# Kernel optimization log

Hardware: AMD Instinct MI355X
Metric: run time of the kernel (lower is better)

## Reference

```python
import jax, jax.numpy as jnp
import numpy as np

N_NODES = 100000


def gcn_conv(x, W, b, src, dst, num_nodes):
    """PyG GCNConv: out = D^{-1/2} (A + I) D^{-1/2} (x W) + b, messages src->dst."""
    h = x @ W  # [N, out]
    # degree with self-loops (edge weight 1)
    deg = jax.ops.segment_sum(jnp.ones(src.shape[0], dtype=x.dtype), dst,
                              num_segments=num_nodes) + 1.0
    dinv = jax.lax.rsqrt(deg)  # [N]
    norm = dinv[src] * dinv[dst]  # [E]
    msg = h[src] * norm[:, None]  # gather + scale, [E, out]
    agg = jax.ops.segment_sum(msg, dst, num_segments=num_nodes)
    # self-loop term: norm_ii = dinv[i]^2
    agg = agg + h * (dinv * dinv)[:, None]
    return agg + b


def setup_inputs() -> dict:
    key = jax.random.key(0)
    ks = jax.random.split(key, 9)
    N, F_in, H1, H2, C = N_NODES, 128, 64, 32, 10
    E = 3200000
    feature = jax.random.normal(ks[0], (N, F_in), dtype=jnp.float32)
    edge_index = jax.random.randint(ks[1], (2, E), 0, N, dtype=jnp.int64)
    def glorot(k, shape):
        lim = np.sqrt(6.0 / (shape[0] + shape[1]))
        return jax.random.uniform(k, shape, jnp.float32, -lim, lim)
    return {
        "feature": feature,
        "edge_index": edge_index,
        "W1": glorot(ks[2], (F_in, H1)),
        "b1": jnp.zeros((H1,), jnp.float32),
        "W2": glorot(ks[3], (H1, H2)),
        "b2": jnp.zeros((H2,), jnp.float32),
        "Wc": glorot(ks[4], (H2, C)),
        "bc": jnp.zeros((C,), jnp.float32),
    }


def reference(feature, edge_index, W1, b1, W2, b2, Wc, bc):
    src, dst = edge_index[0], edge_index[1]
    x = gcn_conv(feature, W1, b1, src, dst, N_NODES)
    x = jax.nn.relu(x)
    # dropout is identity in eval mode
    x = gcn_conv(x, W2, b2, src, dst, N_NODES)
    x = jax.nn.relu(x)
    logits = x @ Wc + bc
    return jax.nn.log_softmax(logits, axis=1)
```

## Files before the change

### kernel.cpp

```cpp
#include <hip/hip_runtime.h>

#define N_NODES 100000
#define F_IN 128
#define H1 64
#define H2 32
#define NCLS 10

#define BS_N 256
#define NBUCK ((N_NODES + BS_N - 1) / BS_N)
#define LCAP 32
#define MCAP 9216
#define OVCAP 6144
#define STCAP 9216
#define BIN_WG 256

typedef _Float16 h2_t __attribute__((ext_vector_type(2)));
typedef _Float16 f16x8 __attribute__((ext_vector_type(8)));
typedef float f32x4 __attribute__((ext_vector_type(4)));

__device__ __forceinline__ float fdot2u(unsigned int u, h2_t sel, float c) {
    return __builtin_amdgcn_fdot2(__builtin_bit_cast(h2_t, u), sel, c, false);
}
__device__ __forceinline__ void accd4(float* a, uint4 v, h2_t lo, h2_t hi) {
    a[0] = fdot2u(v.x, lo, a[0]); a[1] = fdot2u(v.x, hi, a[1]);
    a[2] = fdot2u(v.y, lo, a[2]); a[3] = fdot2u(v.y, hi, a[3]);
    a[4] = fdot2u(v.z, lo, a[4]); a[5] = fdot2u(v.z, hi, a[5]);
    a[6] = fdot2u(v.w, lo, a[6]); a[7] = fdot2u(v.w, hi, a[7]);
}
__device__ __forceinline__ unsigned int pkh(float a, float b) {
    return __builtin_bit_cast(unsigned int, __builtin_amdgcn_cvt_pkrtz(a, b));
}

__global__ __launch_bounds__(512) void bin_kernel(const int* __restrict__ src,
                                                  const int* __restrict__ dst, int E,
                                                  unsigned int* __restrict__ gcur,
                                                  unsigned int* __restrict__ mainr,
                                                  unsigned int* __restrict__ ovcnt,
                                                  unsigned int* __restrict__ ovbuf) {
    __shared__ unsigned int buf[NBUCK][LCAP + 1];
    __shared__ int cnt[NBUCK];
    int tid = threadIdx.x;
    for (int b = tid; b < NBUCK; b += 512) cnt[b] = 0;

    int chunk = (E + gridDim.x - 1) / gridDim.x;
    int e_lo = blockIdx.x * chunk;
    int e_hi = min(e_lo + chunk, E);

    int d[4], s[4];
    #pragma unroll
    for (int k = 0; k < 4; ++k) {
        int e = e_lo + k * 512 + tid;
        d[k] = 0; s[k] = 0;
        if (e < e_hi) { d[k] = dst[e]; s[k] = src[e]; }
    }
    __syncthreads();

    for (int base = e_lo; base < e_hi; base += 2048) {
        #pragma unroll
        for (int k = 0; k < 4; ++k) {
            if (base + k * 512 + tid < e_hi) {
                int b = d[k] >> 8;
                unsigned int en = ((unsigned int)s[k] << 8) | (unsigned int)(d[k] & 255);
                int p = atomicAdd(&cnt[b], 1);
                if (p < LCAP) buf[b][p] = en;
                else {
                    unsigned int op = atomicAdd(&ovcnt[b * 16], 1u);
                    if (op < OVCAP) ovbuf[(size_t)b * OVCAP + op] = en;
                }
            }
        }
        __syncthreads();
        {
            int nb = base + 2048;
            #pragma unroll
            for (int k = 0; k < 4; ++k) {
                int e = nb + k * 512 + tid;
                if (e < e_hi) { d[k] = dst[e]; s[k] = src[e]; }
            }
        }
        for (int b = tid; b < NBUCK; b += 512) {
            int c = cnt[b]; if (c > LCAP) c = LCAP;
            int nf = c & ~15;
            if (nf) {
                unsigned int gb = atomicAdd(&gcur[b * 16], (unsigned int)nf);
                if (gb + (unsigned)nf <= MCAP) {
                    for (int k = 0; k < nf; k += 4) {
                        uint4 v = make_uint4(buf[b][k], buf[b][k + 1],
                                             buf[b][k + 2], buf[b][k + 3]);
                        *(uint4*)&mainr[(size_t)b * MCAP + gb + k] = v;
                    }
                } else {
                    unsigned int op = atomicAdd(&ovcnt[b * 16], (unsigned int)nf);
                    for (int k = 0; k < nf; ++k)
                        if (op + k < OVCAP) ovbuf[(size_t)b * OVCAP + op + k] = buf[b][k];
                }
                int rem = c - nf;
                for (int k = 0; k < rem; ++k) buf[b][k] = buf[b][nf + k];
                cnt[b] = rem;
            } else {
                cnt[b] = c;
            }
        }
        __syncthreads();
    }
    for (int b = tid; b < NBUCK; b += 512) {
        int c = cnt[b]; if (c > LCAP) c = LCAP;
        int nf = c & ~3;
        if (nf) {
            unsigned int gb = atomicAdd(&gcur[b * 16], (unsigned int)nf);
            if (gb + (unsigned)nf <= MCAP) {
                for (int k = 0; k < nf; k += 4) {
                    uint4 v = make_uint4(buf[b][k], buf[b][k + 1],
                                         buf[b][k + 2], buf[b][k + 3]);
                    *(uint4*)&mainr[(size_t)b * MCAP + gb + k] = v;
                }
            } else {
                unsigned int op = atomicAdd(&ovcnt[b * 16], (unsigned int)nf);
                for (int k = 0; k < nf; ++k)
                    if (op + k < OVCAP) ovbuf[(size_t)b * OVCAP + op + k] = buf[b][k];
            }
        }
        int rem = c - nf;
        if (rem) {
            unsigned int ob = atomicAdd(&ovcnt[b * 16], (unsigned int)rem);
            for (int k = 0; k < rem; ++k)
                if (ob + k < OVCAP) ovbuf[(size_t)b * OVCAP + ob + k] = buf[b][nf + k];
        }
    }
}

__global__ __launch_bounds__(512) void build_kernel(const unsigned int* __restrict__ gcur,
                                                    unsigned int* __restrict__ mainr,
                                                    const unsigned int* __restrict__ ovcnt,
                                                    const unsigned int* __restrict__ ovbuf,
                                                    float* __restrict__ dinv,
                                                    int2* __restrict__ row_se) {
    __shared__ unsigned int stage[STCAP];
    __shared__ unsigned int outb[STCAP];
    __shared__ int degl[BS_N];
    __shared__ int rs_l[BS_N];
    __shared__ int curl[BS_N];
    __shared__ int wtot[4];
    int b = blockIdx.x;
    int tid = threadIdx.x;

    int cm = (int)gcur[b * 16]; if (cm > MCAP) cm = MCAP;
    for (int i = tid; i < cm; i += 512) stage[i] = mainr[(size_t)b * MCAP + i];
    int co = (int)ovcnt[b * 16]; if (co > OVCAP) co = OVCAP;
    for (int i = tid; i < co; i += 512) {
        int p = cm + i;
        if (p < STCAP) stage[p] = ovbuf[(size_t)b * OVCAP + i];
    }
    int c = cm + co; if (c > STCAP) c = STCAP;
    if (tid < BS_N) degl[tid] = 0;
    __syncthreads();

    for (int i = tid; i < c; i += 512) atomicAdd(&degl[stage[i] & 255], 1);
    __syncthreads();

    if (tid < BS_N) {
        int lane = tid & 63, w = tid >> 6;
        int d = degl[tid];
        int x = d;
        #pragma unroll
        for (int off = 1; off < 64; off <<= 1) {
            int y = __shfl_up(x, off);
            if (lane >= off) x += y;
        }
        if (lane == 63) wtot[w] = x;
        __syncthreads();
        int pbase = 0;
        #pragma unroll
        for (int k = 0; k < 4; ++k) if (k < w) pbase += wtot[k];
        rs_l[tid] = pbase + x - d;
        curl[tid] = 0;
    } else {
        __syncthreads();
    }
    __syncthreads();

    for (int i = tid; i < c; i += 512) {
        unsigned int en = stage[i];
        int dl = en & 255;
        int p = atomicAdd(&curl[dl], 1);
        outb[rs_l[dl] + p] = en >> 8;
    }
    __syncthreads();
    size_t gbase = (size_t)b * MCAP;
    int c4 = (c + 3) >> 2;
    for (int i = tid; i < c4; i += 512)
        *(uint4*)&mainr[gbase + (size_t)i * 4] = *(const uint4*)&outb[i * 4];

    int node = b * BS_N + tid;
    if (tid < BS_N && node < N_NODES) {
        int deg = degl[tid];
        dinv[node] = rsqrtf((float)deg + 1.0f);
        int rs = (int)gbase + rs_l[tid];
        row_se[node] = make_int2(rs, rs + deg);
    }
}

__global__ __launch_bounds__(256) void gemm1_kernel(const float* __restrict__ X,
                                                    const float* __restrict__ W,
                                                    const float* __restrict__ dinv,
                                                    unsigned short* __restrict__ H) {
    __shared__ union {
        struct {
            _Float16 As[64][136];
            _Float16 Wf[16][64][8];
        } s;
        _Float16 Hs[64][72];
    } u;
    int r0 = blockIdx.x * 64;
    int tid = threadIdx.x;
    for (int i = tid; i < 2048; i += 256) {
        int row = i >> 5, k4 = i & 31;
        int grow = r0 + row;
        float4 v = (grow < N_NODES) ? ((const float4*)X)[(size_t)grow * 32 + k4]
                                    : make_float4(0.f, 0.f, 0.f, 0.f);
        _Float16 t4[4] = {(_Float16)v.x, (_Float16)v.y, (_Float16)v.z, (_Float16)v.w};
        *(uint2*)&u.s.As[row][k4 * 4] = *(uint2*)t4;
    }
    for (int i = tid; i < F_IN * H1; i += 256) {
        int k = i >> 6, col = i & 63;
        u.s.Wf[k >> 3][col][k & 7] = (_Float16)W[i];
    }
    __syncthreads();

    int lane = tid & 63, w = tid >> 6;
    int lr = lane & 15, lkg = lane >> 4;
    f32x4 acc[4] = {{0.f, 0.f, 0.f, 0.f}, {0.f, 0.f, 0.f, 0.f},
                    {0.f, 0.f, 0.f, 0.f}, {0.f, 0.f, 0.f, 0.f}};
    #pragma unroll
    for (int ks = 0; ks < 4; ++ks) {
        f16x8 a = *(const f16x8*)&u.s.As[w * 16 + lr][ks * 32 + lkg * 8];
        #pragma unroll
        for (int nt = 0; nt < 4; ++nt) {
            f16x8 bfr = *(const f16x8*)&u.s.Wf[ks * 4 + lkg][nt * 16 + lr][0];
            acc[nt] = __builtin_amdgcn_mfma_f32_16x16x32_f16(a, bfr, acc[nt], 0, 0, 0);
        }
    }
    __syncthreads();
    float dv[4];
    #pragma unroll
    for (int q = 0; q < 4; ++q) {
        int grow = r0 + w * 16 + lkg * 4 + q;
        dv[q] = (grow < N_NODES) ? dinv[grow] : 0.f;
    }
    #pragma unroll
    for (int nt = 0; nt < 4; ++nt)
        #pragma unroll
        for (int q = 0; q < 4; ++q)
            u.Hs[w * 16 + lkg * 4 + q][nt * 16 + lr] = (_Float16)(acc[nt][q] * dv[q]);
    __syncthreads();
    for (int i = tid; i < 512; i += 256) {
        int row = i >> 3, seg = i & 7;
        int grow = r0 + row;
        if (grow < N_NODES)
            *(uint4*)&H[(size_t)grow * H1 + seg * 8] = *(const uint4*)&u.Hs[row][seg * 8];
    }
}

__global__ __launch_bounds__(256) void gemm2_kernel(const float* __restrict__ X,
                                                    const float* __restrict__ W,
                                                    const float* __restrict__ dinv,
                                                    unsigned short* __restrict__ H) {
    __shared__ float Xs[64][68];
    __shared__ float Ws[H1 * H2];
    int r0 = blockIdx.x * 64;
    const float4* W4 = (const float4*)W;
    float4* Ws4 = (float4*)Ws;
    for (int i = threadIdx.x; i < H1 * H2 / 4; i += 256) Ws4[i] = W4[i];
    for (int it = 0; it < 4; ++it) {
        int idx = threadIdx.x + it * 256;
        int r = idx >> 4, k4 = idx & 15;
        int row = r0 + r;
        float4 v = (row < N_NODES)
            ? ((const float4*)X)[(size_t)row * 16 + k4]
            : make_float4(0.f, 0.f, 0.f, 0.f);
        *(float4*)&Xs[r][k4 * 4] = v;
    }
    __syncthreads();
    int tx = threadIdx.x & 15;
    int ty = threadIdx.x >> 4;
    float acc[4][2] = {};
    #pragma unroll 8
    for (int k = 0; k < 64; ++k) {
        float2 wb = *(const float2*)&Ws[k * H2 + tx * 2];
        float xa0 = Xs[ty * 4 + 0][k];
        float xa1 = Xs[ty * 4 + 1][k];
        float xa2 = Xs[ty * 4 + 2][k];
        float xa3 = Xs[ty * 4 + 3][k];
        acc[0][0] += xa0 * wb.x; acc[0][1] += xa0 * wb.y;
        acc[1][0] += xa1 * wb.x; acc[1][1] += xa1 * wb.y;
        acc[2][0] += xa2 * wb.x; acc[2][1] += xa2 * wb.y;
        acc[3][0] += xa3 * wb.x; acc[3][1] += xa3 * wb.y;
    }
    #pragma unroll
    for (int i = 0; i < 4; ++i) {
        int row = r0 + ty * 4 + i;
        if (row < N_NODES) {
            float dv = dinv[row];
            *(unsigned int*)&H[(size_t)row * H2 + tx * 2] = pkh(acc[i][0] * dv, acc[i][1] * dv);
        }
    }
}

__global__ __launch_bounds__(256) void pull1_kernel(const unsigned short* __restrict__ h,
                                                    const unsigned int* __restrict__ csr,
                                                    const int2* __restrict__ row_se,
                                                    const float* __restrict__ dinv,
                                                    const float* __restrict__ b,
                                                    float* __restrict__ xout) {
    int wave = (blockIdx.x * 256 + threadIdx.x) >> 6;
    int lane = threadIdx.x & 63;
    int g = lane >> 3;
    int sub = lane & 7;
    int i = wave;
    int2 se = row_se[i];
    int e0 = se.x, e1 = se.y;
    int deg = e1 - e0;
    const h2_t selo = {(_Float16)1.0f, (_Float16)0.0f};
    const h2_t sehi = {(_Float16)0.0f, (_Float16)1.0f};
    float acc[8] = {};
    if (deg <= 48) {
        int sidx = (int)csr[e0 + lane];
        int i0 = __shfl(sidx, g);
        int i1 = __shfl(sidx, 8 + g);
        int i2 = __shfl(sidx, 16 + g);
        int i3 = __shfl(sidx, 24 + g);
        int i4 = __shfl(sidx, 32 + g);
        int i5 = __shfl(sidx, 40 + g);
        bool p0 = (g < deg),      p1 = (8 + g < deg),  p2 = (16 + g < deg);
        bool p3 = (24 + g < deg), p4 = (32 + g < deg), p5 = (40 + g < deg);
        uint4 v0 = make_uint4(0u, 0u, 0u, 0u), v1 = v0, v2 = v0, v3 = v0, v4 = v0, v5 = v0;
        if (p0) v0 = *(const uint4*)&h[(size_t)i0 * H1 + sub * 8];
        if (p1) v1 = *(const uint4*)&h[(size_t)i1 * H1 + sub * 8];
        if (p2) v2 = *(const uint4*)&h[(size_t)i2 * H1 + sub * 8];
        if (p3) v3 = *(const uint4*)&h[(size_t)i3 * H1 + sub * 8];
        if (p4) v4 = *(const uint4*)&h[(size_t)i4 * H1 + sub * 8];
        if (p5) v5 = *(const uint4*)&h[(size_t)i5 * H1 + sub * 8];
        if (p0) accd4(acc, v0, selo, sehi);
        if (p1) accd4(acc, v1, selo, sehi);
        if (p2) accd4(acc, v2, selo, sehi);
        if (p3) accd4(acc, v3, selo, sehi);
        if (p4) accd4(acc, v4, selo, sehi);
        if (p5) accd4(acc, v5, selo, sehi);
    } else {
        int e = e0;
        for (; e + 16 <= e1; e += 16) {
            int s0 = csr[e + g];
            int s1 = csr[e + 8 + g];
            uint4 v0 = *(const uint4*)&h[(size_t)s0 * H1 + sub * 8];
            uint4 v1 = *(const uint4*)&h[(size_t)s1 * H1 + sub * 8];
            accd4(acc, v0, selo, sehi);
            accd4(acc, v1, selo, sehi);
        }
        if (e + 8 <= e1) {
            int s = csr[e + g];
            uint4 v = *(const uint4*)&h[(size_t)s * H1 + sub * 8];
            accd4(acc, v, selo, sehi);
            e += 8;
        }
        if (e < e1) {
            int idx = e + g;
            if (idx < e1) {
                int s = csr[idx];
                uint4 v = *(const uint4*)&h[(size_t)s * H1 + sub * 8];
                accd4(acc, v, selo, sehi);
            }
        }
    }
    #pragma unroll
    for (int m = 8; m < 64; m <<= 1) {
        #pragma unroll
        for (int j = 0; j < 8; ++j) acc[j] += __shfl_xor(acc[j], m);
    }
    if (g == 0) {
        float di = dinv[i];
        uint4 sv = *(const uint4*)&h[(size_t)i * H1 + sub * 8];
        accd4(acc, sv, selo, sehi);
        float4 bb0 = *(const float4*)&b[sub * 8];
        float4 bb1 = *(const float4*)&b[sub * 8 + 4];
        float4 o0, o1;
        o0.x = fmaxf(di * acc[0] + bb0.x, 0.0f);
        o0.y = fmaxf(di * acc[1] + bb0.y, 0.0f);
        o0.z = fmaxf(di * acc[2] + bb0.z, 0.0f);
        o0.w = fmaxf(di * acc[3] + bb0.w, 0.0f);
        o1.x = fmaxf(di * acc[4] + bb1.x, 0.0f);
        o1.y = fmaxf(di * acc[5] + bb1.y, 0.0f);
        o1.z = fmaxf(di * acc[6] + bb1.z, 0.0f);
        o1.w = fmaxf(di * acc[7] + bb1.w, 0.0f);
        *(float4*)&xout[(size_t)i * H1 + sub * 8] = o0;
        *(float4*)&xout[(size_t)i * H1 + sub * 8 + 4] = o1;
    }
}

__global__ __launch_bounds__(256) void pull2_kernel(const unsigned short* __restrict__ h,
                                                    const unsigned int* __restrict__ csr,
                                                    const int2* __restrict__ row_se,
                                                    const float* __restrict__ dinv,
                                                    const float* __restrict__ b,
                                                    float* __restrict__ xout) {
    int wave = (blockIdx.x * 256 + threadIdx.x) >> 6;
    int lane = threadIdx.x & 63;
    int g = lane >> 2;
    int sub = lane & 3;
    int i = wave;
    int2 se = row_se[i];
    int e0 = se.x, e1 = se.y;
    int deg = e1 - e0;
    const h2_t selo = {(_Float16)1.0f, (_Float16)0.0f};
    const h2_t sehi = {(_Float16)0.0f, (_Float16)1.0f};
    float acc[8] = {};
    if (deg <= 48) {
        int sidx = (int)csr[e0 + lane];
        int i0 = __shfl(sidx, g);
        int i1 = __shfl(sidx, 16 + g);
        int i2 = __shfl(sidx, 32 + g);
        bool p0 = (g < deg), p1 = (16 + g < deg), p2 = (32 + g < deg);
        uint4 v0 = make_uint4(0u, 0u, 0u, 0u), v1 = v0, v2 = v0;
        if (p0) v0 = *(const uint4*)&h[(size_t)i0 * H2 + sub * 8];
        if (p1) v1 = *(const uint4*)&h[(size_t)i1 * H2 + sub * 8];
        if (p2) v2 = *(const uint4*)&h[(size_t)i2 * H2 + sub * 8];
        if (p0) accd4(acc, v0, selo, sehi);
        if (p1) accd4(acc, v1, selo, sehi);
        if (p2) accd4(acc, v2, selo, sehi);
    } else {
        int e = e0;
        for (; e + 32 <= e1; e += 32) {
            int s0 = csr[e + g];
            int s1 = csr[e + 16 + g];
            uint4 v0 = *(const uint4*)&h[(size_t)s0 * H2 + sub * 8];
            uint4 v1 = *(const uint4*)&h[(size_t)s1 * H2 + sub * 8];
            accd4(acc, v0, selo, sehi);
            accd4(acc, v1, selo, sehi);
        }
        if (e + 16 <= e1) {
            int s = csr[e + g];
            uint4 v = *(const uint4*)&h[(size_t)s * H2 + sub * 8];
            accd4(acc, v, selo, sehi);
            e += 16;
        }
        if (e < e1) {
            int idx = e + g;
            if (idx < e1) {
                int s = csr[idx];
                uint4 v = *(const uint4*)&h[(size_t)s * H2 + sub * 8];
                accd4(acc, v, selo, sehi);
            }
        }
    }
    #pragma unroll
    for (int m = 4; m < 64; m <<= 1) {
        #pragma unroll
        for (int j = 0; j < 8; ++j) acc[j] += __shfl_xor(acc[j], m);
    }
    if (g == 0) {
        float di = dinv[i];
        uint4 sv = *(const uint4*)&h[(size_t)i * H2 + sub * 8];
        accd4(acc, sv, selo, sehi);
        float4 bb0 = *(const float4*)&b[sub * 8];
        float4 bb1 = *(const float4*)&b[sub * 8 + 4];
        float4 o0, o1;
        o0.x = fmaxf(di * acc[0] + bb0.x, 0.0f);
        o0.y = fmaxf(di * acc[1] + bb0.y, 0.0f);
        o0.z = fmaxf(di * acc[2] + bb0.z, 0.0f);
        o0.w = fmaxf(di * acc[3] + bb0.w, 0.0f);
        o1.x = fmaxf(di * acc[4] + bb1.x, 0.0f);
        o1.y = fmaxf(di * acc[5] + bb1.y, 0.0f);
        o1.z = fmaxf(di * acc[6] + bb1.z, 0.0f);
        o1.w = fmaxf(di * acc[7] + bb1.w, 0.0f);
        *(float4*)&xout[(size_t)i * H2 + sub * 8] = o0;
        *(float4*)&xout[(size_t)i * H2 + sub * 8 + 4] = o1;
    }
}

__global__ __launch_bounds__(256) void final_kernel(const float* __restrict__ X2,
                                                    const float* __restrict__ Wc,
                                                    const float* __restrict__ bc,
                                                    float* __restrict__ out) {
    __shared__ float Ws[H2 * NCLS];
    __shared__ float bs[NCLS];
    for (int idx = threadIdx.x; idx < H2 * NCLS; idx += 256) Ws[idx] = Wc[idx];
    if (threadIdx.x < NCLS) bs[threadIdx.x] = bc[threadIdx.x];
    __syncthreads();
    int i = blockIdx.x * blockDim.x + threadIdx.x;
    if (i >= N_NODES) return;
    float x[H2];
    #pragma unroll
    for (int k = 0; k < H2; ++k) x[k] = X2[(size_t)i * H2 + k];
    float lg[NCLS];
    #pragma unroll
    for (int c = 0; c < NCLS; ++c) {
        float acc = bs[c];
        #pragma unroll
        for (int k = 0; k < H2; ++k) acc += x[k] * Ws[k * NCLS + c];
        lg[c] = acc;
    }
    float m = lg[0];
    #pragma unroll
    for (int c = 1; c < NCLS; ++c) m = fmaxf(m, lg[c]);
    float s = 0.0f;
    #pragma unroll
    for (int c = 0; c < NCLS; ++c) s += expf(lg[c] - m);
    float lse = m + logf(s);
    #pragma unroll
    for (int c = 0; c < NCLS; ++c) out[(size_t)i * NCLS + c] = lg[c] - lse;
}

extern "C" void kernel_launch(void* const* d_in, const int* in_sizes, int n_in,
                              void* d_out, int out_size, void* d_ws, size_t ws_size,
                              hipStream_t stream) {
    const float* feature = (const float*)d_in[0];
    const int*   eidx    = (const int*)d_in[1];
    const float* W1      = (const float*)d_in[2];
    const float* b1      = (const float*)d_in[3];
    const float* W2      = (const float*)d_in[4];
    const float* b2      = (const float*)d_in[5];
    const float* Wc      = (const float*)d_in[6];
    const float* bc      = (const float*)d_in[7];
    float* out = (float*)d_out;

    const int E = in_sizes[1] / 2;
    const int* src = eidx;
    const int* dst = eidx + E;

    float*          ws        = (float*)d_ws;
    float*          dinv      = ws;
    int2*           row_se    = (int2*)(dinv + N_NODES);
    unsigned int*   gcur      = (unsigned int*)(row_se + N_NODES);
    unsigned int*   ovcnt     = gcur + (size_t)NBUCK * 16;
    unsigned int*   ovbuf     = ovcnt + (size_t)NBUCK * 16;
    unsigned int*   mainr     = ovbuf + (size_t)NBUCK * OVCAP;
    unsigned short* h1b       = (unsigned short*)(mainr + (size_t)NBUCK * MCAP);
    float*          x1        = (float*)(h1b + (size_t)N_NODES * H1);
    unsigned short* h2b       = h1b;
    float*          x2        = x1;

    hipMemsetAsync(gcur, 0, (size_t)NBUCK * 32 * sizeof(unsigned int), stream);
    bin_kernel<<<BIN_WG, 512, 0, stream>>>(src, dst, E, gcur, mainr, ovcnt, ovbuf);
    build_kernel<<<NBUCK, 512, 0, stream>>>(gcur, mainr, ovcnt, ovbuf, dinv, row_se);

    gemm1_kernel<<<(N_NODES + 63) / 64, 256, 0, stream>>>(feature, W1, dinv, h1b);
    {
        unsigned int grid = (unsigned int)(((size_t)N_NODES * 64 + 255) / 256);
        pull1_kernel<<<grid, 256, 0, stream>>>(h1b, mainr, row_se, dinv, b1, x1);
    }

    gemm2_kernel<<<(N_NODES + 63) / 64, 256, 0, stream>>>(x1, W2, dinv, h2b);
    {
        unsigned int grid = (unsigned int)(((size_t)N_NODES * 64 + 255) / 256);
        pull2_kernel<<<grid, 256, 0, stream>>>(h2b, mainr, row_se, dinv, b2, x2);
    }

    final_kernel<<<(N_NODES + 255) / 256, 256, 0, stream>>>(x2, Wc, bc, out);
}
```

Baseline: 272.8 us.

## Process two nodes per wave in pull1 and fuse classifier into pull2

pull1 now has each wavefront aggregate two destination nodes. It interleaves their neighbour gathers so more loads are in flight, and the grid is halved. pull2 absorbs the final linear layer and log-softmax: it stages each node's hidden vector in shared memory and computes the logits within the block. That removes the x2 write and reread and one kernel launch. The costs are extra block-level syncs and shared-memory traffic in pull2, and more register pressure in pull1.

```diff
diff --git a/kernel.cpp b/kernel.cpp
--- a/kernel.cpp
+++ b/kernel.cpp
@@ -306,6 +306,51 @@
     }
 }
 
+#define GEN1(e0v, e1v, acc) do {                                               \
+    int e = (e0v);                                                             \
+    for (; e + 16 <= (e1v); e += 16) {                                         \
+        int s0 = csr[e + g];                                                   \
+        int s1 = csr[e + 8 + g];                                               \
+        uint4 v0 = *(const uint4*)&h[(size_t)s0 * H1 + sub * 8];               \
+        uint4 v1 = *(const uint4*)&h[(size_t)s1 * H1 + sub * 8];               \
+        accd4(acc, v0, selo, sehi);                                            \
+        accd4(acc, v1, selo, sehi);                                            \
+    }                                                                          \
+    if (e + 8 <= (e1v)) {                                                      \
+        int s0 = csr[e + g];                                                   \
+        uint4 v0 = *(const uint4*)&h[(size_t)s0 * H1 + sub * 8];               \
+        accd4(acc, v0, selo, sehi);                                            \
+        e += 8;                                                                \
+    }                                                                          \
+    if (e < (e1v)) {                                                           \
+        int idx = e + g;                                                       \
+        if (idx < (e1v)) {                                                     \
+            int s0 = csr[idx];                                                 \
+            uint4 v0 = *(const uint4*)&h[(size_t)s0 * H1 + sub * 8];           \
+            accd4(acc, v0, selo, sehi);                                        \
+        }                                                                      \
+    }                                                                          \
+} while (0)
+
+#define EPI1(nodei, acc) do {                                                  \
+    float di = dinv[nodei];                                                    \
+    uint4 sv = *(const uint4*)&h[(size_t)(nodei) * H1 + sub * 8];              \
+    accd4(acc, sv, selo, sehi);                                                \
+    float4 bb0 = *(const float4*)&b[sub * 8];                                  \
+    float4 bb1 = *(const float4*)&b[sub * 8 + 4];                              \
+    float4 o0, o1;                                                             \
+    o0.x = fmaxf(di * (acc)[0] + bb0.x, 0.0f);                                 \
+    o0.y = fmaxf(di * (acc)[1] + bb0.y, 0.0f);                                 \
+    o0.z = fmaxf(di * (acc)[2] + bb0.z, 0.0f);                                 \
+    o0.w = fmaxf(di * (acc)[3] + bb0.w, 0.0f);                                 \
+    o1.x = fmaxf(di * (acc)[4] + bb1.x, 0.0f);                                 \
+    o1.y = fmaxf(di * (acc)[5] + bb1.y, 0.0f);                                 \
+    o1.z = fmaxf(di * (acc)[6] + bb1.z, 0.0f);                                 \
+    o1.w = fmaxf(di * (acc)[7] + bb1.w, 0.0f);                                 \
+    *(float4*)&xout[(size_t)(nodei) * H1 + sub * 8] = o0;                      \
+    *(float4*)&xout[(size_t)(nodei) * H1 + sub * 8 + 4] = o1;                  \
+} while (0)
+
 __global__ __launch_bounds__(256) void pull1_kernel(const unsigned short* __restrict__ h,
                                                     const unsigned int* __restrict__ csr,
                                                     const int2* __restrict__ row_se,
@@ -316,83 +361,67 @@
     int lane = threadIdx.x & 63;
     int g = lane >> 3;
     int sub = lane & 7;
-    int i = wave;
-    int2 se = row_se[i];
-    int e0 = se.x, e1 = se.y;
-    int deg = e1 - e0;
+    int iA = wave * 2, iB = iA + 1;
+    int4 se2 = *(const int4*)&row_se[iA];
+    int e0A = se2.x, e1A = se2.y, e0B = se2.z, e1B = se2.w;
+    int degA = e1A - e0A, degB = e1B - e0B;
     const h2_t selo = {(_Float16)1.0f, (_Float16)0.0f};
     const h2_t sehi = {(_Float16)0.0f, (_Float16)1.0f};
-    float acc[8] = {};
-    if (deg <= 48) {
-        int sidx = (int)csr[e0 + lane];
-        int i0 = __shfl(sidx, g);
-        int i1 = __shfl(sidx, 8 + g);
-        int i2 = __shfl(sidx, 16 + g);
-        int i3 = __shfl(sidx, 24 + g);
-        int i4 = __shfl(sidx, 32 + g);
-        int i5 = __shfl(sidx, 40 + g);
-        bool p0 = (g < deg),      p1 = (8 + g < deg),  p2 = (16 + g < deg);
-        bool p3 = (24 + g < deg), p4 = (32 + g < deg), p5 = (40 + g < deg);
-        uint4 v0 = make_uint4(0u, 0u, 0u, 0u), v1 = v0, v2 = v0, v3 = v0, v4 = v0, v5 = v0;
-        if (p0) v0 = *(const uint4*)&h[(size_t)i0 * H1 + sub * 8];
-        if (p1) v1 = *(const uint4*)&h[(size_t)i1 * H1 + sub * 8];
-        if (p2) v2 = *(const uint4*)&h[(size_t)i2 * H1 + sub * 8];
-        if (p3) v3 = *(const uint4*)&h[(size_t)i3 * H1 + sub * 8];
-        if (p4) v4 = *(const uint4*)&h[(size_t)i4 * H1 + sub * 8];
-        if (p5) v5 = *(const uint4*)&h[(size_t)i5 * H1 + sub * 8];
-        if (p0) accd4(acc, v0, selo, sehi);
-        if (p1) accd4(acc, v1, selo, sehi);
-        if (p2) accd4(acc, v2, selo, sehi);
-        if (p3) accd4(acc, v3, selo, sehi);
-        if (p4) accd4(acc, v4, selo, sehi);
-        if (p5) accd4(acc, v5, selo, sehi);
+    float accA[8] = {}, accB[8] = {};
+    if (degA <= 48 && degB <= 48) {
+        int sA = (int)csr[e0A + lane];
+        int sB = (int)csr[e0B + lane];
+        int a0 = __shfl(sA, g),      a1 = __shfl(sA, 8 + g),  a2 = __shfl(sA, 16 + g);
+        int a3 = __shfl(sA, 24 + g), a4 = __shfl(sA, 32 + g), a5 = __shfl(sA, 40 + g);
+        int b0 = __shfl(sB, g),      b1 = __shfl(sB, 8 + g),  b2 = __shfl(sB, 16 + g);
+        int b3 = __shfl(sB, 24 + g), b4 = __shfl(sB, 32 + g), b5 = __shfl(sB, 40 + g);
+        bool pa0 = (g < degA),      pa1 = (8 + g < degA),  pa2 = (16 + g < degA);
+        bool pa3 = (24 + g < degA), pa4 = (32 + g < degA), pa5 = (40 + g < degA);
+        bool pb0 = (g < degB),      pb1 = (8 + g < degB),  pb2 = (16 + g < degB);
+        bool pb3 = (24 + g < degB), pb4 = (32 + g < degB), pb5 = (40 + g < degB);
+        uint4 z = make_uint4(0u, 0u, 0u, 0u);
+        uint4 va0 = z, va1 = z, va2 = z, va3 = z, va4 = z, va5 = z;
+        uint4 vb0 = z, vb1 = z, vb2 = z, vb3 = z, vb4 = z, vb5 = z;
+        if (pa0) va0 = *(const uint4*)&h[(size_t)a0 * H1 + sub * 8];
+        if (pb0) vb0 = *(const uint4*)&h[(size_t)b0 * H1 + sub * 8];
+        if (pa1) va1 = *(const uint4*)&h[(size_t)a1 * H1 + sub * 8];
+        if (pb1) vb1 = *(const uint4*)&h[(size_t)b1 * H1 + sub * 8];
+        if (pa2) va2 = *(const uint4*)&h[(size_t)a2 * H1 + sub * 8];
+        if (pb2) vb2 = *(const uint4*)&h[(size_t)b2 * H1 + sub * 8];
+        if (pa3) va3 = *(const uint4*)&h[(size_t)a3 * H1 + sub * 8];
+        if (pb3) vb3 = *(const uint4*)&h[(size_t)b3 * H1 + sub * 8];
+        if (pa4) va4 = *(const uint4*)&h[(size_t)a4 * H1 + sub * 8];
+        if (pb4) vb4 = *(const uint4*)&h[(size_t)b4 * H1 + sub * 8];
+        if (pa5) va5 = *(const uint4*)&h[(size_t)a5 * H1 + sub * 8];
+        if (pb5) vb5 = *(const uint4*)&h[(size_t)b5 * H1 + sub * 8];
+        if (pa0) accd4(accA, va0, selo, sehi);
+        if (pa1) accd4(accA, va1, selo, sehi);
+        if (pa2) accd4(accA, va2, selo, sehi);
+        if (pa3) accd4(accA, va3, selo, sehi);
+        if (pa4) accd4(accA, va4, selo, sehi);
+        if (pa5) accd4(accA, va5, selo, sehi);
+        if (pb0) accd4(accB, vb0, selo, sehi);
+        if (pb1) accd4(accB, vb1, selo, sehi);
+        if (pb2) accd4(accB, vb2, selo, sehi);
+        if (pb3) accd4(accB, vb3, selo, sehi);
+        if (pb4) accd4(accB, vb4, selo, sehi);
+        if (pb5) accd4(accB, vb5, selo, sehi);
     } else {
-        int e = e0;
-        for (; e + 16 <= e1; e += 16) {
-            int s0 = csr[e + g];
-            int s1 = csr[e + 8 + g];
-            uint4 v0 = *(const uint4*)&h[(size_t)s0 * H1 + sub * 8];
-            uint4 v1 = *(const uint4*)&h[(size_t)s1 * H1 + sub * 8];
-            accd4(acc, v0, selo, sehi);
-            accd4(acc, v1, selo, sehi);
-        }
-        if (e + 8 <= e1) {
-            int s = csr[e + g];
-            uint4 v = *(const uint4*)&h[(size_t)s * H1 + sub * 8];
-            accd4(acc, v, selo, sehi);
-            e += 8;
-        }
-        if (e < e1) {
-            int idx = e + g;
-            if (idx < e1) {
-                int s = csr[idx];
-                uint4 v = *(const uint4*)&h[(size_t)s * H1 + sub * 8];
-                accd4(acc, v, selo, sehi);
-            }
-        }
+        GEN1(e0A, e1A, accA);
+        GEN1(e0B, e1B, accB);
     }
     #pragma unroll
     for (int m = 8; m < 64; m <<= 1) {
         #pragma unroll
-        for (int j = 0; j < 8; ++j) acc[j] += __shfl_xor(acc[j], m);
-    }
-    if (g == 0) {
-        float di = dinv[i];
-        uint4 sv = *(const uint4*)&h[(size_t)i * H1 + sub * 8];
-        accd4(acc, sv, selo, sehi);
-        float4 bb0 = *(const float4*)&b[sub * 8];
-        float4 bb1 = *(const float4*)&b[sub * 8 + 4];
-        float4 o0, o1;
-        o0.x = fmaxf(di * acc[0] + bb0.x, 0.0f);
-        o0.y = fmaxf(di * acc[1] + bb0.y, 0.0f);
-        o0.z = fmaxf(di * acc[2] + bb0.z, 0.0f);
-        o0.w = fmaxf(di * acc[3] + bb0.w, 0.0f);
-        o1.x = fmaxf(di * acc[4] + bb1.x, 0.0f);
-        o1.y = fmaxf(di * acc[5] + bb1.y, 0.0f);
-        o1.z = fmaxf(di * acc[6] + bb1.z, 0.0f);
-        o1.w = fmaxf(di * acc[7] + bb1.w, 0.0f);
-        *(float4*)&xout[(size_t)i * H1 + sub * 8] = o0;
-        *(float4*)&xout[(size_t)i * H1 + sub * 8 + 4] = o1;
+        for (int j = 0; j < 8; ++j) {
+            accA[j] += __shfl_xor(accA[j], m);
+            accB[j] += __shfl_xor(accB[j], m);
+        }
+    }
+    if (lane < 8) {
+        EPI1(iA, accA);
+    } else if (lane < 16) {
+        EPI1(iB, accB);
     }
 }
 
@@ -401,12 +430,24 @@
                                                     const int2* __restrict__ row_se,
                                                     const float* __restrict__ dinv,
                                                     const float* __restrict__ b,
-                                                    float* __restrict__ xout) {
-    int wave = (blockIdx.x * 256 + threadIdx.x) >> 6;
-    int lane = threadIdx.x & 63;
+                                                    const float* __restrict__ Wc,
+                                                    const float* __restrict__ bc,
+                                                    float* __restrict__ out) {
+    __shared__ float WsL[H2 * NCLS];
+    __shared__ float bsL[NCLS];
+    __shared__ float xsh[4][H2];
+    __shared__ float lgl[4][NCLS];
+    __shared__ float lsel[4];
+    int tid = threadIdx.x;
+    for (int idx = tid; idx < H2 * NCLS; idx += 256) WsL[idx] = Wc[idx];
+    if (tid < NCLS) bsL[tid] = bc[tid];
+    __syncthreads();
+
+    int w = tid >> 6;
+    int i = blockIdx.x * 4 + w;
+    int lane = tid & 63;
     int g = lane >> 2;
     int sub = lane & 3;
-    int i = wave;
     int2 se = row_se[i];
     int e0 = se.x, e1 = se.y;
     int deg = e1 - e0;
@@ -462,51 +503,38 @@
         accd4(acc, sv, selo, sehi);
         float4 bb0 = *(const float4*)&b[sub * 8];
         float4 bb1 = *(const float4*)&b[sub * 8 + 4];
-        float4 o0, o1;
-        o0.x = fmaxf(di * acc[0] + bb0.x, 0.0f);
-        o0.y = fmaxf(di * acc[1] + bb0.y, 0.0f);
-        o0.z = fmaxf(di * acc[2] + bb0.z, 0.0f);
-        o0.w = fmaxf(di * acc[3] + bb0.w, 0.0f);
-        o1.x = fmaxf(di * acc[4] + bb1.x, 0.0f);
-        o1.y = fmaxf(di * acc[5] + bb1.y, 0.0f);
-        o1.z = fmaxf(di * acc[6] + bb1.z, 0.0f);
-        o1.w = fmaxf(di * acc[7] + bb1.w, 0.0f);
-        *(float4*)&xout[(size_t)i * H2 + sub * 8] = o0;
-        *(float4*)&xout[(size_t)i * H2 + sub * 8 + 4] = o1;
-    }
-}
-
-__global__ __launch_bounds__(256) void final_kernel(const float* __restrict__ X2,
-                                                    const float* __restrict__ Wc,
-                                                    const float* __restrict__ bc,
-                                                    float* __restrict__ out) {
-    __shared__ float Ws[H2 * NCLS];
-    __shared__ float bs[NCLS];
-    for (int idx = threadIdx.x; idx < H2 * NCLS; idx += 256) Ws[idx] = Wc[idx];
-    if (threadIdx.x < NCLS) bs[threadIdx.x] = bc[threadIdx.x];
-    __syncthreads();
-    int i = blockIdx.x * blockDim.x + threadIdx.x;
-    if (i >= N_NODES) return;
-    float x[H2];
-    #pragma unroll
-    for (int k = 0; k < H2; ++k) x[k] = X2[(size_t)i * H2 + k];
-    float lg[NCLS];
-    #pragma unroll
-    for (int c = 0; c < NCLS; ++c) {
-        float acc = bs[c];
-        #pragma unroll
-        for (int k = 0; k < H2; ++k) acc += x[k] * Ws[k * NCLS + c];
-        lg[c] = acc;
-    }
-    float m = lg[0];
-    #pragma unroll
-    for (int c = 1; c < NCLS; ++c) m = fmaxf(m, lg[c]);
-    float s = 0.0f;
-    #pragma unroll
-    for (int c = 0; c < NCLS; ++c) s += expf(lg[c] - m);
-    float lse = m + logf(s);
-    #pragma unroll
-    for (int c = 0; c < NCLS; ++c) out[(size_t)i * NCLS + c] = lg[c] - lse;
+        xsh[w][sub * 8 + 0] = fmaxf(di * acc[0] + bb0.x, 0.0f);
+        xsh[w][sub * 8 + 1] = fmaxf(di * acc[1] + bb0.y, 0.0f);
+        xsh[w][sub * 8 + 2] = fmaxf(di * acc[2] + bb0.z, 0.0f);
+        xsh[w][sub * 8 + 3] = fmaxf(di * acc[3] + bb0.w, 0.0f);
+        xsh[w][sub * 8 + 4] = fmaxf(di * acc[4] + bb1.x, 0.0f);
+        xsh[w][sub * 8 + 5] = fmaxf(di * acc[5] + bb1.y, 0.0f);
+        xsh[w][sub * 8 + 6] = fmaxf(di * acc[6] + bb1.z, 0.0f);
+        xsh[w][sub * 8 + 7] = fmaxf(di * acc[7] + bb1.w, 0.0f);
+    }
+    __syncthreads();
+    if (tid < 4 * NCLS) {
+        int nd = tid / NCLS, c2 = tid % NCLS;
+        float a2 = bsL[c2];
+        #pragma unroll
+        for (int k = 0; k < H2; ++k) a2 += xsh[nd][k] * WsL[k * NCLS + c2];
+        lgl[nd][c2] = a2;
+    }
+    __syncthreads();
+    if (tid < 4) {
+        float m2 = lgl[tid][0];
+        #pragma unroll
+        for (int c2 = 1; c2 < NCLS; ++c2) m2 = fmaxf(m2, lgl[tid][c2]);
+        float s2 = 0.f;
+        #pragma unroll
+        for (int c2 = 0; c2 < NCLS; ++c2) s2 += expf(lgl[tid][c2] - m2);
+        lsel[tid] = m2 + logf(s2);
+    }
+    __syncthreads();
+    if (tid < 4 * NCLS) {
+        int nd = tid / NCLS, c2 = tid % NCLS;
+        out[(size_t)(blockIdx.x * 4 + nd) * NCLS + c2] = lgl[nd][c2] - lsel[nd];
+    }
 }
 
 extern "C" void kernel_launch(void* const* d_in, const int* in_sizes, int n_in,
@@ -536,23 +564,14 @@
     unsigned short* h1b       = (unsigned short*)(mainr + (size_t)NBUCK * MCAP);
     float*          x1        = (float*)(h1b + (size_t)N_NODES * H1);
     unsigned short* h2b       = h1b;
-    float*          x2        = x1;
 
     hipMemsetAsync(gcur, 0, (size_t)NBUCK * 32 * sizeof(unsigned int), stream);
     bin_kernel<<<BIN_WG, 512, 0, stream>>>(src, dst, E, gcur, mainr, ovcnt, ovbuf);
     build_kernel<<<NBUCK, 512, 0, stream>>>(gcur, mainr, ovcnt, ovbuf, dinv, row_se);
 
     gemm1_kernel<<<(N_NODES + 63) / 64, 256, 0, stream>>>(feature, W1, dinv, h1b);
-    {
-        unsigned int grid = (unsigned int)(((size_t)N_NODES * 64 + 255) / 256);
-        pull1_kernel<<<grid, 256, 0, stream>>>(h1b, mainr, row_se, dinv, b1, x1);
-    }
+    pull1_kernel<<<12500, 256, 0, stream>>>(h1b, mainr, row_se, dinv, b1, x1);
 
     gemm2_kernel<<<(N_NODES + 63) / 64, 256, 0, stream>>>(x1, W2, dinv, h2b);
-    {
-        unsigned int grid = (unsigned int)(((size_t)N_NODES * 64 + 255) / 256);
-        pull2_kernel<<<grid, 256, 0, stream>>>(h2b, mainr, row_se, dinv, b2, x2);
-    }
-
-    final_kernel<<<(N_NODES + 255) / 256, 256, 0, stream>>>(x2, Wc, bc, out);
-}
+    pull2_kernel<<<N_NODES / 4, 256, 0, stream>>>(h2b, mainr, row_se, dinv, b2, Wc, bc, out);
+}
```

Result: slower. 287.8 us (+5.5%).

## Split layer-2 pull aggregation into two source-range passes for cache locality

Applied to the files above, without the earlier changes.

The layer-2 gather-aggregate runs as two passes. Each pass gathers only neighbours whose source index falls in one half of the node range, so the gathered h rows for that half (about 3.2 MB in fp16) stay in cache. The first pass writes float partial sums to a new buffer, and the second pass adds them back before the bias, ReLU and scaling. In exchange every pass re-reads the CSR and row ranges, and a full fp32 partial tensor is written and read. The unrolled 32-edge loop is also replaced by a simpler 16-edge loop.

```diff
diff --git a/kernel.cpp b/kernel.cpp
--- a/kernel.cpp
+++ b/kernel.cpp
@@ -5,6 +5,7 @@
 #define H1 64
 #define H2 32
 #define NCLS 10
+#define SPLIT 50000
 
 #define BS_N 256
 #define NBUCK ((N_NODES + BS_N - 1) / BS_N)
@@ -396,12 +397,10 @@
     }
 }
 
-__global__ __launch_bounds__(256) void pull2_kernel(const unsigned short* __restrict__ h,
-                                                    const unsigned int* __restrict__ csr,
-                                                    const int2* __restrict__ row_se,
-                                                    const float* __restrict__ dinv,
-                                                    const float* __restrict__ b,
-                                                    float* __restrict__ xout) {
+__global__ __launch_bounds__(256) void pull2a_kernel(const unsigned short* __restrict__ h,
+                                                     const unsigned int* __restrict__ csr,
+                                                     const int2* __restrict__ row_se,
+                                                     float* __restrict__ part) {
     int wave = (blockIdx.x * 256 + threadIdx.x) >> 6;
     int lane = threadIdx.x & 63;
     int g = lane >> 2;
@@ -418,7 +417,9 @@
         int i0 = __shfl(sidx, g);
         int i1 = __shfl(sidx, 16 + g);
         int i2 = __shfl(sidx, 32 + g);
-        bool p0 = (g < deg), p1 = (16 + g < deg), p2 = (32 + g < deg);
+        bool p0 = (g < deg) && (i0 < SPLIT);
+        bool p1 = (16 + g < deg) && (i1 < SPLIT);
+        bool p2 = (32 + g < deg) && (i2 < SPLIT);
         uint4 v0 = make_uint4(0u, 0u, 0u, 0u), v1 = v0, v2 = v0;
         if (p0) v0 = *(const uint4*)&h[(size_t)i0 * H2 + sub * 8];
         if (p1) v1 = *(const uint4*)&h[(size_t)i1 * H2 + sub * 8];
@@ -427,27 +428,14 @@
         if (p1) accd4(acc, v1, selo, sehi);
         if (p2) accd4(acc, v2, selo, sehi);
     } else {
-        int e = e0;
-        for (; e + 32 <= e1; e += 32) {
-            int s0 = csr[e + g];
-            int s1 = csr[e + 16 + g];
-            uint4 v0 = *(const uint4*)&h[(size_t)s0 * H2 + sub * 8];
-            uint4 v1 = *(const uint4*)&h[(size_t)s1 * H2 + sub * 8];
-            accd4(acc, v0, selo, sehi);
-            accd4(acc, v1, selo, sehi);
-        }
-        if (e + 16 <= e1) {
-            int s = csr[e + g];
-            uint4 v = *(const uint4*)&h[(size_t)s * H2 + sub * 8];
-            accd4(acc, v, selo, sehi);
-            e += 16;
-        }
-        if (e < e1) {
+        for (int e = e0; e < e1; e += 16) {
             int idx = e + g;
             if (idx < e1) {
                 int s = csr[idx];
-                uint4 v = *(const uint4*)&h[(size_t)s * H2 + sub * 8];
-                accd4(acc, v, selo, sehi);
+                if (s < SPLIT) {
+                    uint4 v = *(const uint4*)&h[(size_t)s * H2 + sub * 8];
+                    accd4(acc, v, selo, sehi);
+                }
             }
         }
     }
@@ -457,9 +445,77 @@
         for (int j = 0; j < 8; ++j) acc[j] += __shfl_xor(acc[j], m);
     }
     if (g == 0) {
+        if (i < SPLIT) {
+            uint4 sv = *(const uint4*)&h[(size_t)i * H2 + sub * 8];
+            accd4(acc, sv, selo, sehi);
+        }
+        *(float4*)&part[(size_t)i * H2 + sub * 8] =
+            make_float4(acc[0], acc[1], acc[2], acc[3]);
+        *(float4*)&part[(size_t)i * H2 + sub * 8 + 4] =
+            make_float4(acc[4], acc[5], acc[6], acc[7]);
+    }
+}
+
+__global__ __launch_bounds__(256) void pull2b_kernel(const unsigned short* __restrict__ h,
+                                                     const unsigned int* __restrict__ csr,
+                                                     const int2* __restrict__ row_se,
+                                                     const float* __restrict__ dinv,
+                                                     const float* __restrict__ b,
+                                                     const float* __restrict__ part,
+                                                     float* __restrict__ xout) {
+    int wave = (blockIdx.x * 256 + threadIdx.x) >> 6;
+    int lane = threadIdx.x & 63;
+    int g = lane >> 2;
+    int sub = lane & 3;
+    int i = wave;
+    int2 se = row_se[i];
+    int e0 = se.x, e1 = se.y;
+    int deg = e1 - e0;
+    const h2_t selo = {(_Float16)1.0f, (_Float16)0.0f};
+    const h2_t sehi = {(_Float16)0.0f, (_Float16)1.0f};
+    float acc[8] = {};
+    if (deg <= 48) {
+        int sidx = (int)csr[e0 + lane];
+        int i0 = __shfl(sidx, g);
+        int i1 = __shfl(sidx, 16 + g);
+        int i2 = __shfl(sidx, 32 + g);
+        bool p0 = (g < deg) && (i0 >= SPLIT);
+        bool p1 = (16 + g < deg) && (i1 >= SPLIT);
+        bool p2 = (32 + g < deg) && (i2 >= SPLIT);
+        uint4 v0 = make_uint4(0u, 0u, 0u, 0u), v1 = v0, v2 = v0;
+        if (p0) v0 = *(const uint4*)&h[(size_t)i0 * H2 + sub * 8];
+        if (p1) v1 = *(const uint4*)&h[(size_t)i1 * H2 + sub * 8];
+        if (p2) v2 = *(const uint4*)&h[(size_t)i2 * H2 + sub * 8];
+        if (p0) accd4(acc, v0, selo, sehi);
+        if (p1) accd4(acc, v1, selo, sehi);
+        if (p2) accd4(acc, v2, selo, sehi);
+    } else {
+        for (int e = e0; e < e1; e += 16) {
+            int idx = e + g;
+            if (idx < e1) {
+                int s = csr[idx];
+                if (s >= SPLIT) {
+                    uint4 v = *(const uint4*)&h[(size_t)s * H2 + sub * 8];
+                    accd4(acc, v, selo, sehi);
+                }
+            }
+        }
+    }
+    #pragma unroll
+    for (int m = 4; m < 64; m <<= 1) {
+        #pragma unroll
+        for (int j = 0; j < 8; ++j) acc[j] += __shfl_xor(acc[j], m);
+    }
+    if (g == 0) {
+        if (i >= SPLIT) {
+            uint4 sv = *(const uint4*)&h[(size_t)i * H2 + sub * 8];
+            accd4(acc, sv, selo, sehi);
+        }
+        float4 pr0 = *(const float4*)&part[(size_t)i * H2 + sub * 8];
+        float4 pr1 = *(const float4*)&part[(size_t)i * H2 + sub * 8 + 4];
+        acc[0] += pr0.x; acc[1] += pr0.y; acc[2] += pr0.z; acc[3] += pr0.w;
+        acc[4] += pr1.x; acc[5] += pr1.y; acc[6] += pr1.z; acc[7] += pr1.w;
         float di = dinv[i];
-        uint4 sv = *(const uint4*)&h[(size_t)i * H2 + sub * 8];
-        accd4(acc, sv, selo, sehi);
         float4 bb0 = *(const float4*)&b[sub * 8];
         float4 bb1 = *(const float4*)&b[sub * 8 + 4];
         float4 o0, o1;
@@ -537,6 +593,7 @@
     float*          x1        = (float*)(h1b + (size_t)N_NODES * H1);
     unsigned short* h2b       = h1b;
     float*          x2        = x1;
+    float*          part      = x1 + (size_t)N_NODES * H2;
 
     hipMemsetAsync(gcur, 0, (size_t)NBUCK * 32 * sizeof(unsigned int), stream);
     bin_kernel<<<BIN_WG, 512, 0, stream>>>(src, dst, E, gcur, mainr, ovcnt, ovbuf);
@@ -551,7 +608,8 @@
     gemm2_kernel<<<(N_NODES + 63) / 64, 256, 0, stream>>>(x1, W2, dinv, h2b);
     {
         unsigned int grid = (unsigned int)(((size_t)N_NODES * 64 + 255) / 256);
-        pull2_kernel<<<grid, 256, 0, stream>>>(h2b, mainr, row_se, dinv, b2, x2);
+        pull2a_kernel<<<grid, 256, 0, stream>>>(h2b, mainr, row_se, part);
+        pull2b_kernel<<<grid, 256, 0, stream>>>(h2b, mainr, row_se, dinv, b2, part, x2);
     }
 
     final_kernel<<<(N_NODES + 255) / 256, 256, 0, stream>>>(x2, Wc, bc, out);
```

After: 314.5 us. 1.15x slower.

## Fuse layer-2 GEMM into layer-1 aggregation epilogue

Applied to the files above, without the earlier changes.

Removes the separate gemm2 kernel. The pull1 kernel now stages a transposed W2 in shared memory and, after aggregating each node, applies bias, ReLU, the 64x32 projection and dinv scaling, writing fp16 h2 directly. This avoids writing and re-reading the fp32 intermediate x1 and saves one launch. It costs redundant per-lane projection math, a per-block W2 load and an extra shuffle reduction in the aggregation kernel.

```diff
diff --git a/kernel.cpp b/kernel.cpp
--- a/kernel.cpp
+++ b/kernel.cpp
@@ -261,57 +261,20 @@
     }
 }
 
-__global__ __launch_bounds__(256) void gemm2_kernel(const float* __restrict__ X,
-                                                    const float* __restrict__ W,
-                                                    const float* __restrict__ dinv,
-                                                    unsigned short* __restrict__ H) {
-    __shared__ float Xs[64][68];
-    __shared__ float Ws[H1 * H2];
-    int r0 = blockIdx.x * 64;
-    const float4* W4 = (const float4*)W;
-    float4* Ws4 = (float4*)Ws;
-    for (int i = threadIdx.x; i < H1 * H2 / 4; i += 256) Ws4[i] = W4[i];
-    for (int it = 0; it < 4; ++it) {
-        int idx = threadIdx.x + it * 256;
-        int r = idx >> 4, k4 = idx & 15;
-        int row = r0 + r;
-        float4 v = (row < N_NODES)
-            ? ((const float4*)X)[(size_t)row * 16 + k4]
-            : make_float4(0.f, 0.f, 0.f, 0.f);
-        *(float4*)&Xs[r][k4 * 4] = v;
-    }
-    __syncthreads();
-    int tx = threadIdx.x & 15;
-    int ty = threadIdx.x >> 4;
-    float acc[4][2] = {};
-    #pragma unroll 8
-    for (int k = 0; k < 64; ++k) {
-        float2 wb = *(const float2*)&Ws[k * H2 + tx * 2];
-        float xa0 = Xs[ty * 4 + 0][k];
-        float xa1 = Xs[ty * 4 + 1][k];
-        float xa2 = Xs[ty * 4 + 2][k];
-        float xa3 = Xs[ty * 4 + 3][k];
-        acc[0][0] += xa0 * wb.x; acc[0][1] += xa0 * wb.y;
-        acc[1][0] += xa1 * wb.x; acc[1][1] += xa1 * wb.y;
-        acc[2][0] += xa2 * wb.x; acc[2][1] += xa2 * wb.y;
-        acc[3][0] += xa3 * wb.x; acc[3][1] += xa3 * wb.y;
-    }
-    #pragma unroll
-    for (int i = 0; i < 4; ++i) {
-        int row = r0 + ty * 4 + i;
-        if (row < N_NODES) {
-            float dv = dinv[row];
-            *(unsigned int*)&H[(size_t)row * H2 + tx * 2] = pkh(acc[i][0] * dv, acc[i][1] * dv);
-        }
-    }
-}
-
 __global__ __launch_bounds__(256) void pull1_kernel(const unsigned short* __restrict__ h,
                                                     const unsigned int* __restrict__ csr,
                                                     const int2* __restrict__ row_se,
                                                     const float* __restrict__ dinv,
                                                     const float* __restrict__ b,
-                                                    float* __restrict__ xout) {
+                                                    const float* __restrict__ W2,
+                                                    unsigned short* __restrict__ h2out) {
+    __shared__ float W2t[H2 * H1];
+    for (int idx = threadIdx.x; idx < H1 * H2; idx += 256) {
+        int k = idx >> 5, c = idx & 31;
+        W2t[c * H1 + k] = W2[idx];
+    }
+    __syncthreads();
+
     int wave = (blockIdx.x * 256 + threadIdx.x) >> 6;
     int lane = threadIdx.x & 63;
     int g = lane >> 3;
@@ -376,23 +339,37 @@
         #pragma unroll
         for (int j = 0; j < 8; ++j) acc[j] += __shfl_xor(acc[j], m);
     }
-    if (g == 0) {
-        float di = dinv[i];
-        uint4 sv = *(const uint4*)&h[(size_t)i * H1 + sub * 8];
-        accd4(acc, sv, selo, sehi);
-        float4 bb0 = *(const float4*)&b[sub * 8];
-        float4 bb1 = *(const float4*)&b[sub * 8 + 4];
-        float4 o0, o1;
-        o0.x = fmaxf(di * acc[0] + bb0.x, 0.0f);
-        o0.y = fmaxf(di * acc[1] + bb0.y, 0.0f);
-        o0.z = fmaxf(di * acc[2] + bb0.z, 0.0f);
-        o0.w = fmaxf(di * acc[3] + bb0.w, 0.0f);
-        o1.x = fmaxf(di * acc[4] + bb1.x, 0.0f);
-        o1.y = fmaxf(di * acc[5] + bb1.y, 0.0f);
-        o1.z = fmaxf(di * acc[6] + bb1.z, 0.0f);
-        o1.w = fmaxf(di * acc[7] + bb1.w, 0.0f);
-        *(float4*)&xout[(size_t)i * H1 + sub * 8] = o0;
-        *(float4*)&xout[(size_t)i * H1 + sub * 8 + 4] = o1;
+    float di = dinv[i];
+    uint4 sv = *(const uint4*)&h[(size_t)i * H1 + sub * 8];
+    accd4(acc, sv, selo, sehi);
+    float4 bb0 = *(const float4*)&b[sub * 8];
+    float4 bb1 = *(const float4*)&b[sub * 8 + 4];
+    float x0 = fmaxf(di * acc[0] + bb0.x, 0.0f);
+    float x1 = fmaxf(di * acc[1] + bb0.y, 0.0f);
+    float x2 = fmaxf(di * acc[2] + bb0.z, 0.0f);
+    float x3 = fmaxf(di * acc[3] + bb0.w, 0.0f);
+    float x4 = fmaxf(di * acc[4] + bb1.x, 0.0f);
+    float x5 = fmaxf(di * acc[5] + bb1.y, 0.0f);
+    float x6 = fmaxf(di * acc[6] + bb1.z, 0.0f);
+    float x7 = fmaxf(di * acc[7] + bb1.w, 0.0f);
+    float p[4];
+    #pragma unroll
+    for (int cc = 0; cc < 4; ++cc) {
+        const float* wr = &W2t[(g * 4 + cc) * H1 + sub * 8];
+        float4 wa = *(const float4*)wr;
+        float4 wb = *(const float4*)(wr + 4);
+        p[cc] = x0 * wa.x + x1 * wa.y + x2 * wa.z + x3 * wa.w
+              + x4 * wb.x + x5 * wb.y + x6 * wb.z + x7 * wb.w;
+    }
+    #pragma unroll
+    for (int m = 1; m <= 4; m <<= 1) {
+        #pragma unroll
+        for (int cc = 0; cc < 4; ++cc) p[cc] += __shfl_xor(p[cc], m);
+    }
+    if (sub == 0) {
+        unsigned int lo = pkh(p[0] * di, p[1] * di);
+        unsigned int hi = pkh(p[2] * di, p[3] * di);
+        *(uint2*)&h2out[(size_t)i * H2 + g * 4] = make_uint2(lo, hi);
     }
 }
 
@@ -534,9 +511,8 @@
     unsigned int*   ovbuf     = ovcnt + (size_t)NBUCK * 16;
     unsigned int*   mainr     = ovbuf + (size_t)NBUCK * OVCAP;
     unsigned short* h1b       = (unsigned short*)(mainr + (size_t)NBUCK * MCAP);
-    float*          x1        = (float*)(h1b + (size_t)N_NODES * H1);
-    unsigned short* h2b       = h1b;
-    float*          x2        = x1;
+    unsigned short* h2b       = h1b + (size_t)N_NODES * H1;
+    float*          x2        = (float*)h1b;
 
     hipMemsetAsync(gcur, 0, (size_t)NBUCK * 32 * sizeof(unsigned int), stream);
     bin_kernel<<<BIN_WG, 512, 0, stream>>>(src, dst, E, gcur, mainr, ovcnt, ovbuf);
@@ -545,10 +521,9 @@
     gemm1_kernel<<<(N_NODES + 63) / 64, 256, 0, stream>>>(feature, W1, dinv, h1b);
     {
         unsigned int grid = (unsigned int)(((size_t)N_NODES * 64 + 255) / 256);
-        pull1_kernel<<<grid, 256, 0, stream>>>(h1b, mainr, row_se, dinv, b1, x1);
-    }
-
-    gemm2_kernel<<<(N_NODES + 63) / 64, 256, 0, stream>>>(x1, W2, dinv, h2b);
+        pull1_kernel<<<grid, 256, 0, stream>>>(h1b, mainr, row_se, dinv, b1, W2, h2b);
+    }
+
     {
         unsigned int grid = (unsigned int)(((size_t)N_NODES * 64 + 255) / 256);
         pull2_kernel<<<grid, 256, 0, stream>>>(h2b, mainr, row_se, dinv, b2, x2);
```

Measured after the change: 348.9 us. 27.9% more time.
